# Kernel tuning notes

Measured on AMD Instinct MI355X. Metric: run time of the kernel, lower is better.

The kernel has to match this reference:

```python
import jax, jax.numpy as jnp
import numpy as np
import math

IN_CH = 1024
OUT_CH = 1024
QK_DIM = 512
NHEADS = 8
NDIM = QK_DIM // NHEADS  # 64 per-head qk dim
VDIM = OUT_CH // NHEADS  # 128 per-head value dim
SCALE = 1.0 / math.sqrt(NDIM)


def setup_inputs() -> dict:
    key = jax.random.key(0)
    ks = jax.random.split(key, 7)
    B, N = 4, 2048
    x = jax.random.normal(ks[0], (B, N, IN_CH), dtype=jnp.float32)
    # Linear weights stored as [in, out] so y = x @ W + b
    s_in = 1.0 / math.sqrt(IN_CH)
    Wq = jax.random.uniform(ks[1], (IN_CH, QK_DIM), jnp.float32, -s_in, s_in)
    bq = jax.random.uniform(ks[2], (QK_DIM,), jnp.float32, -s_in, s_in)
    Wk = jax.random.uniform(ks[3], (IN_CH, QK_DIM), jnp.float32, -s_in, s_in)
    bk = jax.random.uniform(ks[4], (QK_DIM,), jnp.float32, -s_in, s_in)
    Wv = jax.random.uniform(ks[5], (IN_CH, OUT_CH), jnp.float32, -s_in, s_in)
    bv = jax.random.uniform(ks[6], (OUT_CH,), jnp.float32, -s_in, s_in)
    return {"x": x, "Wq": Wq, "bq": bq, "Wk": Wk, "bk": bk, "Wv": Wv, "bv": bv}


def reference(x, Wq, bq, Wk, bk, Wv, bv):
    B, N, C = x.shape
    Q = (x @ Wq + bq).reshape(B, N, NHEADS, NDIM)
    K = (x @ Wk + bk).reshape(B, N, NHEADS, NDIM)
    V = (x @ Wv + bv).reshape(B, N, NHEADS, VDIM)
    # scores: [B, H, N, N]
    scores = jnp.einsum("bnhd,bmhd->bhnm", Q, K) * SCALE
    attn = jax.nn.softmax(scores, axis=-1)
    # message: [B, N, H, VDIM] -> [B, N, OUT_CH]
    msg = jnp.einsum("bhnm,bmhv->bnhv", attn, V)
    return msg.reshape(B, N, OUT_CH)
```

## Files before the change

### kernel.cpp

```cpp
#include <hip/hip_runtime.h>
#include <hip/hip_bf16.h>
#include <math.h>


using bf16 = __hip_bfloat16;
typedef __attribute__((ext_vector_type(8))) short short8;
typedef __attribute__((ext_vector_type(4))) float f32x4;
typedef __attribute__((ext_vector_type(16))) float f32x16;
typedef __attribute__((ext_vector_type(2))) unsigned int uintx2;

#define C2 0.18033688011112042f

__device__ __forceinline__ void async_ld16(const void* g, void* l) {
  __builtin_amdgcn_global_load_lds(
      (const __attribute__((address_space(1))) unsigned int*)g,
      (__attribute__((address_space(3))) unsigned int*)l, 16, 0, 0);
}

__global__ __launch_bounds__(256) void convert_x(const float* __restrict__ x,
                                                 bf16* __restrict__ xb)
{
  const int i = (blockIdx.x * 256 + threadIdx.x) * 8;
  const float4 a = *(const float4*)(x + i);
  const float4 b = *(const float4*)(x + i + 4);
  union { bf16 h[8]; short8 s; } u;
  u.h[0] = __float2bfloat16(a.x); u.h[1] = __float2bfloat16(a.y);
  u.h[2] = __float2bfloat16(a.z); u.h[3] = __float2bfloat16(a.w);
  u.h[4] = __float2bfloat16(b.x); u.h[5] = __float2bfloat16(b.y);
  u.h[6] = __float2bfloat16(b.z); u.h[7] = __float2bfloat16(b.w);
  *(short8*)(xb + i) = u.s;
}

__global__ __launch_bounds__(256) void transpose_weights(
    const float* __restrict__ Wq, const float* __restrict__ Wk,
    const float* __restrict__ Wv, bf16* __restrict__ Wt)
{
  __shared__ __align__(16) bf16 t[32][33];
  const int i0 = blockIdx.x * 32;
  const int o0 = blockIdx.y * 32;
  const int tx = threadIdx.x & 31, ty = threadIdx.x >> 5;
#pragma unroll
  for (int s = 0; s < 32; s += 8) {
    const int i = i0 + ty + s;
    const int o = o0 + tx;
    const float w = (o < 512)  ? Wq[(size_t)i * 512 + o]
                  : (o < 1024) ? Wk[(size_t)i * 512 + (o - 512)]
                               : Wv[(size_t)i * 1024 + (o - 1024)];
    t[ty + s][tx] = __float2bfloat16(w);
  }
  __syncthreads();
#pragma unroll
  for (int s = 0; s < 32; s += 8)
    Wt[(size_t)(o0 + ty + s) * 1024 + i0 + tx] = t[tx][ty + s];
}

__global__ __launch_bounds__(256, 2) void qkv_gemm(
    const bf16* __restrict__ xb, const bf16* __restrict__ Wt,
    const float* __restrict__ bq, const float* __restrict__ bk,
    const float* __restrict__ bv, bf16* __restrict__ QKV)
{
  __shared__ __align__(16) bf16 As[128 * 64];
  __shared__ __align__(16) bf16 Bs[128 * 64];
  const int tid = threadIdx.x;
  const int w = tid >> 6, lane = tid & 63, quad = lane >> 4, l16 = lane & 15;
  const int m0 = blockIdx.y * 128, n0 = blockIdx.x * 128;
  const int wm = (w >> 1) * 64, wn = (w & 1) * 64;
  f32x4 acc[4][4];
  const f32x4 z4 = {0.f, 0.f, 0.f, 0.f};
#pragma unroll
  for (int mi = 0; mi < 4; ++mi)
#pragma unroll
    for (int ni = 0; ni < 4; ++ni) acc[mi][ni] = z4;

  for (int k0 = 0; k0 < 1024; k0 += 64) {
    __syncthreads();
#pragma unroll
    for (int it = 0; it < 4; ++it) {
      const int L = it * 256 + tid;
      const int row = L >> 3;
      const int c16 = (L & 7) ^ (row & 7);
      async_ld16(xb + (size_t)(m0 + row) * 1024 + k0 + c16 * 8, &As[L * 8]);
      async_ld16(Wt + (size_t)(n0 + row) * 1024 + k0 + c16 * 8, &Bs[L * 8]);
    }
    __syncthreads();
#pragma unroll
    for (int kk = 0; kk < 2; ++kk) {
      short8 af[4], bfr[4];
#pragma unroll
      for (int mi = 0; mi < 4; ++mi) {
        const int row = wm + mi * 16 + l16;
        const int p = ((kk << 2) | quad) ^ (row & 7);
        af[mi] = *(const short8*)&As[row * 64 + p * 8];
      }
#pragma unroll
      for (int ni = 0; ni < 4; ++ni) {
        const int row = wn + ni * 16 + l16;
        const int p = ((kk << 2) | quad) ^ (row & 7);
        bfr[ni] = *(const short8*)&Bs[row * 64 + p * 8];
      }
#pragma unroll
      for (int mi = 0; mi < 4; ++mi)
#pragma unroll
        for (int ni = 0; ni < 4; ++ni)
          acc[mi][ni] = __builtin_amdgcn_mfma_f32_16x16x32_bf16(af[mi], bfr[ni], acc[mi][ni], 0, 0, 0);
    }
  }
#pragma unroll
  for (int ni = 0; ni < 4; ++ni) {
    const int colg = n0 + wn + ni * 16 + l16;
    const float bias = colg < 512 ? bq[colg]
                     : (colg < 1024 ? bk[colg - 512] : bv[colg - 1024]);
    const float scl = (colg >= 512 && colg < 1024) ? C2 : 1.0f;
#pragma unroll
    for (int mi = 0; mi < 4; ++mi)
#pragma unroll
      for (int reg = 0; reg < 4; ++reg) {
        const int rowg = m0 + wm + mi * 16 + quad * 4 + reg;
        QKV[(size_t)rowg * 2048 + colg] = __float2bfloat16((acc[mi][ni][reg] + bias) * scl);
      }
  }
}

__global__ __launch_bounds__(256) void transpose_v(
    const bf16* __restrict__ QKV, bf16* __restrict__ Vt)
{
  __shared__ __align__(16) bf16 t[32][33];
  const int r0 = blockIdx.x * 32;
  const int c0 = blockIdx.y * 32;
  const int tx = threadIdx.x & 31, ty = threadIdx.x >> 5;
#pragma unroll
  for (int s = 0; s < 32; s += 8)
    t[ty + s][tx] = QKV[(size_t)(r0 + ty + s) * 2048 + 1024 + c0 + tx];
  __syncthreads();
#pragma unroll
  for (int s = 0; s < 32; s += 8)
    Vt[(size_t)(c0 + ty + s) * 8192 + r0 + tx] = t[tx][ty + s];
}

__global__ __launch_bounds__(256, 2) void flash_attn(
    const bf16* __restrict__ QKV, const bf16* __restrict__ Vt, float* __restrict__ out)
{
  __shared__ __align__(16) bf16 smem[3 * 12288];
  char* smemc = (char*)smem;
  const int tid = threadIdx.x;
  const int w = tid >> 6, lane = tid & 63, l31 = lane & 31, hi = lane >> 5;
  const int q0 = blockIdx.x * 128;
  const int h  = blockIdx.y;
  const size_t tb = (size_t)blockIdx.z * 2048;

  short8 qf[4];
  const int qrow = w * 32 + l31;
  const bf16* qptr = QKV + (tb + q0 + qrow) * 2048 + h * 64 + hi * 8;
#pragma unroll
  for (int dd = 0; dd < 4; ++dd)
    qf[dd] = *(const short8*)(qptr + dd * 16);

  int adr[4];
#pragma unroll
  for (int i = 0; i < 4; ++i)
    adr[i] = l31 * 128 + (((2 * i + hi) ^ (l31 & 7)) * 16);

  const bf16* kg[2]; int kldo[2];
#pragma unroll
  for (int i = 0; i < 2; ++i) {
    const int L = i * 256 + tid, row = L >> 3, c = (L & 7) ^ (row & 7);
    kg[i] = QKV + (tb + row) * 2048 + 512 + h * 64 + c * 8;
    kldo[i] = L * 16;
  }
  const bf16* vg[4]; int vldo[4];
#pragma unroll
  for (int i = 0; i < 4; ++i) {
    const int L = i * 256 + tid, row = L >> 3, c = (L & 7) ^ (row & 7);
    vg[i] = Vt + (size_t)(h * 128 + row) * 8192 + tb + c * 8;
    vldo[i] = L * 16;
  }

  f32x16 O[4];
#pragma unroll
  for (int t = 0; t < 4; ++t)
#pragma unroll
    for (int e = 0; e < 16; ++e) O[t][e] = 0.f;
  f32x16 Z;
#pragma unroll
  for (int e = 0; e < 16; ++e) Z[e] = 0.f;
  float2 rs; rs.x = 0.f; rs.y = 0.f;

#define STAGE(B) do {                                                        \
  _Pragma("unroll") for (int i = 0; i < 2; ++i) {                            \
    async_ld16(kg[i], smemc + (B) * 24576 + kldo[i]); kg[i] += 131072; }     \
  _Pragma("unroll") for (int i = 0; i < 4; ++i) {                            \
    async_ld16(vg[i], smemc + (B) * 24576 + 8192 + vldo[i]); vg[i] += 64; }  \
} while (0)

#define SOFTPV(B, KT, SV) do {                                               \
  unsigned int pk[8];                                                        \
  _Pragma("unroll") for (int dw = 0; dw < 8; ++dw) {                         \
    const float e0 = exp2f(SV[2 * dw]);                                      \
    const float e1 = exp2f(SV[2 * dw + 1]);                                  \
    rs.x += e0; rs.y += e1;                                                  \
    union { bf16 hh[2]; unsigned int u; } cc;                                \
    cc.hh[0] = __float2bfloat16(e0); cc.hh[1] = __float2bfloat16(e1);        \
    pk[dw] = cc.u; }                                                         \
  _Pragma("unroll") for (int half = 0; half < 2; ++half) {                   \
    const int kc = 2 * (KT) + half; const int b4 = half * 4;                 \
    const uintx2 s0 = __builtin_amdgcn_permlane32_swap(pk[b4], pk[b4 + 2], false, false);     \
    const uintx2 s1 = __builtin_amdgcn_permlane32_swap(pk[b4 + 1], pk[b4 + 3], false, false); \
    union { unsigned int d[4]; short8 v; } pf;                               \
    pf.d[0] = s0.x; pf.d[1] = s1.x; pf.d[2] = s0.y; pf.d[3] = s1.y;          \
    _Pragma("unroll") for (int vt = 0; vt < 4; ++vt) {                       \
      const short8 vf = *(const short8*)(smemc + (B) * 24576 + 8192 + vt * 4096 + adr[kc]); \
      O[vt] = __builtin_amdgcn_mfma_f32_32x32x16_bf16(vf, pf.v, O[vt], 0, 0, 0); } }        \
} while (0)

#define COMPUTE(B) do {                                                      \
  __builtin_amdgcn_s_setprio(1);                                            \
  short8 kf; f32x16 S0, S1;                                                  \
  kf = *(const short8*)(smemc + (B) * 24576 + adr[0]);                       \
  S0 = __builtin_amdgcn_mfma_f32_32x32x16_bf16(kf, qf[0], Z, 0, 0, 0);       \
  kf = *(const short8*)(smemc + (B) * 24576 + adr[1]);                       \
  S0 = __builtin_amdgcn_mfma_f32_32x32x16_bf16(kf, qf[1], S0, 0, 0, 0);      \
  kf = *(const short8*)(smemc + (B) * 24576 + adr[2]);                       \
  S0 = __builtin_amdgcn_mfma_f32_32x32x16_bf16(kf, qf[2], S0, 0, 0, 0);      \
  kf = *(const short8*)(smemc + (B) * 24576 + adr[3]);                       \
  S0 = __builtin_amdgcn_mfma_f32_32x32x16_bf16(kf, qf[3], S0, 0, 0, 0);      \
  kf = *(const short8*)(smemc + (B) * 24576 + 4096 + adr[0]);                \
  S1 = __builtin_amdgcn_mfma_f32_32x32x16_bf16(kf, qf[0], Z, 0, 0, 0);       \
  kf = *(const short8*)(smemc + (B) * 24576 + 4096 + adr[1]);                \
  S1 = __builtin_amdgcn_mfma_f32_32x32x16_bf16(kf, qf[1], S1, 0, 0, 0);      \
  kf = *(const short8*)(smemc + (B) * 24576 + 4096 + adr[2]);                \
  S1 = __builtin_amdgcn_mfma_f32_32x32x16_bf16(kf, qf[2], S1, 0, 0, 0);      \
  kf = *(const short8*)(smemc + (B) * 24576 + 4096 + adr[3]);                \
  S1 = __builtin_amdgcn_mfma_f32_32x32x16_bf16(kf, qf[3], S1, 0, 0, 0);      \
  SOFTPV(B, 0, S0);                                                          \
  SOFTPV(B, 1, S1);                                                          \
  __builtin_amdgcn_s_setprio(0);                                            \
} while (0)

#define PIPE_SYNC6 do {                                                      \
  asm volatile("s_waitcnt vmcnt(6)" ::: "memory");                           \
  __builtin_amdgcn_s_barrier();                                              \
  __builtin_amdgcn_sched_barrier(0);                                         \
} while (0)

  STAGE(0); STAGE(1);
  PIPE_SYNC6;
  for (int u = 0; u < 10; ++u) {
    STAGE(2); COMPUTE(0); PIPE_SYNC6;
    STAGE(0); COMPUTE(1); PIPE_SYNC6;
    STAGE(1); COMPUTE(2); PIPE_SYNC6;
  }
  COMPUTE(0);
  asm volatile("s_waitcnt vmcnt(0)" ::: "memory");
  __builtin_amdgcn_s_barrier();
  __builtin_amdgcn_sched_barrier(0);
  COMPUTE(1);

#undef STAGE
#undef SOFTPV
#undef COMPUTE
#undef PIPE_SYNC6

  float l_run = rs.x + rs.y;
  l_run += __shfl_xor(l_run, 32, 64);

  const float inv_l = 1.0f / l_run;
  float* tbuf = (float*)smem;
  const int qg = tid >> 1;
  const int part = tid & 1;
  for (int vt = 0; vt < 4; ++vt) {
    __syncthreads();
#pragma unroll
    for (int e = 0; e < 16; ++e) {
      const int vl = (e & 3) + 8 * (e >> 2) + 4 * hi;
      tbuf[vl * 132 + w * 32 + l31] = O[vt][e] * inv_l;
    }
    __syncthreads();
    float* dst = out + (tb + q0 + qg) * 1024 + h * 128 + vt * 32 + part * 16;
#pragma unroll
    for (int i = 0; i < 4; ++i) {
      float4 v4;
      v4.x = tbuf[(part * 16 + 4 * i + 0) * 132 + qg];
      v4.y = tbuf[(part * 16 + 4 * i + 1) * 132 + qg];
      v4.z = tbuf[(part * 16 + 4 * i + 2) * 132 + qg];
      v4.w = tbuf[(part * 16 + 4 * i + 3) * 132 + qg];
      *(float4*)(dst + 4 * i) = v4;
    }
  }
}

extern "C" void kernel_launch(void* const* d_in, const int* in_sizes, int n_in,
                              void* d_out, int out_size, void* d_ws, size_t ws_size,
                              hipStream_t stream) {
  const float* x  = (const float*)d_in[0];
  const float* Wq = (const float*)d_in[1];
  const float* bq = (const float*)d_in[2];
  const float* Wk = (const float*)d_in[3];
  const float* bk = (const float*)d_in[4];
  const float* Wv = (const float*)d_in[5];
  const float* bv = (const float*)d_in[6];
  float* out = (float*)d_out;

  char* ws = (char*)d_ws;
  bf16* QKV = (bf16*)ws;
  bf16* Vt  = (bf16*)(ws + 33554432);
  bf16* Wt  = (bf16*)(ws + 33554432 + 16777216);
  bf16* xb  = (bf16*)(ws + 33554432 + 16777216 + 4194304);

  convert_x<<<dim3(4096), 256, 0, stream>>>(x, xb);
  transpose_weights<<<dim3(32, 64), 256, 0, stream>>>(Wq, Wk, Wv, Wt);
  qkv_gemm<<<dim3(16, 64), 256, 0, stream>>>(xb, Wt, bq, bk, bv, QKV);
  transpose_v<<<dim3(256, 32), 256, 0, stream>>>(QKV, Vt);
  flash_attn<<<dim3(16, 8, 4), 256, 0, stream>>>(QKV, Vt, out);
}
```

Before: 226.9 us.

## Split attention over two key halves with combine pass and leaner LDS pipeline

```diff
diff --git a/kernel.cpp b/kernel.cpp
--- a/kernel.cpp
+++ b/kernel.cpp
@@ -57,7 +57,7 @@
 __global__ __launch_bounds__(256, 2) void qkv_gemm(
     const bf16* __restrict__ xb, const bf16* __restrict__ Wt,
     const float* __restrict__ bq, const float* __restrict__ bk,
-    const float* __restrict__ bv, bf16* __restrict__ QKV)
+    const float* __restrict__ bv, bf16* __restrict__ QK, bf16* __restrict__ Vtmp)
 {
   __shared__ __align__(16) bf16 As[128 * 64];
   __shared__ __align__(16) bf16 Bs[128 * 64];
@@ -105,6 +105,8 @@
           acc[mi][ni] = __builtin_amdgcn_mfma_f32_16x16x32_bf16(af[mi], bfr[ni], acc[mi][ni], 0, 0, 0);
     }
   }
+  bf16* dst = (n0 < 1024) ? QK : Vtmp;
+  const int cofs = (n0 < 1024) ? 0 : 1024;
 #pragma unroll
   for (int ni = 0; ni < 4; ++ni) {
     const int colg = n0 + wn + ni * 16 + l16;
@@ -116,13 +118,13 @@
 #pragma unroll
       for (int reg = 0; reg < 4; ++reg) {
         const int rowg = m0 + wm + mi * 16 + quad * 4 + reg;
-        QKV[(size_t)rowg * 2048 + colg] = __float2bfloat16((acc[mi][ni][reg] + bias) * scl);
+        dst[(size_t)rowg * 1024 + (colg - cofs)] = __float2bfloat16((acc[mi][ni][reg] + bias) * scl);
       }
   }
 }
 
 __global__ __launch_bounds__(256) void transpose_v(
-    const bf16* __restrict__ QKV, bf16* __restrict__ Vt)
+    const bf16* __restrict__ Vtmp, bf16* __restrict__ Vt)
 {
   __shared__ __align__(16) bf16 t[32][33];
   const int r0 = blockIdx.x * 32;
@@ -130,27 +132,32 @@
   const int tx = threadIdx.x & 31, ty = threadIdx.x >> 5;
 #pragma unroll
   for (int s = 0; s < 32; s += 8)
-    t[ty + s][tx] = QKV[(size_t)(r0 + ty + s) * 2048 + 1024 + c0 + tx];
+    t[ty + s][tx] = Vtmp[(size_t)(r0 + ty + s) * 1024 + c0 + tx];
   __syncthreads();
 #pragma unroll
   for (int s = 0; s < 32; s += 8)
     Vt[(size_t)(c0 + ty + s) * 8192 + r0 + tx] = t[tx][ty + s];
 }
 
-__global__ __launch_bounds__(256, 2) void flash_attn(
-    const bf16* __restrict__ QKV, const bf16* __restrict__ Vt, float* __restrict__ out)
-{
-  __shared__ __align__(16) bf16 smem[3 * 12288];
+__global__ __launch_bounds__(256, 4) void flash_attn(
+    const bf16* __restrict__ QK, const bf16* __restrict__ Vt,
+    float* __restrict__ out, float* __restrict__ P1,
+    float* __restrict__ l0, float* __restrict__ l1)
+{
+  __shared__ __align__(16) bf16 smem[16384];
   char* smemc = (char*)smem;
   const int tid = threadIdx.x;
   const int w = tid >> 6, lane = tid & 63, l31 = lane & 31, hi = lane >> 5;
   const int q0 = blockIdx.x * 128;
   const int h  = blockIdx.y;
-  const size_t tb = (size_t)blockIdx.z * 2048;
+  const int b  = blockIdx.z >> 1;
+  const int half_ = blockIdx.z & 1;
+  const int kbase = half_ * 1024;
+  const size_t tb = (size_t)b * 2048;
 
   short8 qf[4];
   const int qrow = w * 32 + l31;
-  const bf16* qptr = QKV + (tb + q0 + qrow) * 2048 + h * 64 + hi * 8;
+  const bf16* qptr = QK + (tb + q0 + qrow) * 1024 + h * 64 + hi * 8;
 #pragma unroll
   for (int dd = 0; dd < 4; ++dd)
     qf[dd] = *(const short8*)(qptr + dd * 16);
@@ -164,16 +171,17 @@
 #pragma unroll
   for (int i = 0; i < 2; ++i) {
     const int L = i * 256 + tid, row = L >> 3, c = (L & 7) ^ (row & 7);
-    kg[i] = QKV + (tb + row) * 2048 + 512 + h * 64 + c * 8;
+    kg[i] = QK + (tb + kbase + row) * 1024 + 512 + h * 64 + c * 8;
     kldo[i] = L * 16;
   }
   const bf16* vg[4]; int vldo[4];
 #pragma unroll
   for (int i = 0; i < 4; ++i) {
     const int L = i * 256 + tid, row = L >> 3, c = (L & 7) ^ (row & 7);
-    vg[i] = Vt + (size_t)(h * 128 + row) * 8192 + tb + c * 8;
+    vg[i] = Vt + (size_t)(h * 128 + row) * 8192 + tb + kbase + c * 8;
     vldo[i] = L * 16;
   }
+  int4 vr[4];
 
   f32x16 O[4];
 #pragma unroll
@@ -185,14 +193,16 @@
   for (int e = 0; e < 16; ++e) Z[e] = 0.f;
   float2 rs; rs.x = 0.f; rs.y = 0.f;
 
-#define STAGE(B) do {                                                        \
-  _Pragma("unroll") for (int i = 0; i < 2; ++i) {                            \
-    async_ld16(kg[i], smemc + (B) * 24576 + kldo[i]); kg[i] += 131072; }     \
-  _Pragma("unroll") for (int i = 0; i < 4; ++i) {                            \
-    async_ld16(vg[i], smemc + (B) * 24576 + 8192 + vldo[i]); vg[i] += 64; }  \
-} while (0)
-
-#define SOFTPV(B, KT, SV) do {                                               \
+#define VLOAD() do { _Pragma("unroll") for (int i = 0; i < 4; ++i) {         \
+    vr[i] = *(const int4*)vg[i]; vg[i] += 64; } } while (0)
+
+#define VSTORE() do { _Pragma("unroll") for (int i = 0; i < 4; ++i)          \
+    *(int4*)(smemc + 16384 + vldo[i]) = vr[i]; } while (0)
+
+#define KSTAGE(PAR) do { _Pragma("unroll") for (int i = 0; i < 2; ++i) {     \
+    async_ld16(kg[i], smemc + (PAR) * 8192 + kldo[i]); kg[i] += 65536; } } while (0)
+
+#define SOFTPV(KT, SV) do {                                                  \
   unsigned int pk[8];                                                        \
   _Pragma("unroll") for (int dw = 0; dw < 8; ++dw) {                         \
     const float e0 = exp2f(SV[2 * dw]);                                      \
@@ -208,62 +218,76 @@
     union { unsigned int d[4]; short8 v; } pf;                               \
     pf.d[0] = s0.x; pf.d[1] = s1.x; pf.d[2] = s0.y; pf.d[3] = s1.y;          \
     _Pragma("unroll") for (int vt = 0; vt < 4; ++vt) {                       \
-      const short8 vf = *(const short8*)(smemc + (B) * 24576 + 8192 + vt * 4096 + adr[kc]); \
-      O[vt] = __builtin_amdgcn_mfma_f32_32x32x16_bf16(vf, pf.v, O[vt], 0, 0, 0); } }        \
+      const short8 vf = *(const short8*)(smemc + 16384 + vt * 4096 + adr[kc]); \
+      O[vt] = __builtin_amdgcn_mfma_f32_32x32x16_bf16(vf, pf.v, O[vt], 0, 0, 0); } } \
 } while (0)
 
-#define COMPUTE(B) do {                                                      \
-  __builtin_amdgcn_s_setprio(1);                                            \
+#define COMPUTE(PAR) do {                                                    \
+  __builtin_amdgcn_s_setprio(1);                                             \
   short8 kf; f32x16 S0, S1;                                                  \
-  kf = *(const short8*)(smemc + (B) * 24576 + adr[0]);                       \
+  kf = *(const short8*)(smemc + (PAR) * 8192 + adr[0]);                      \
   S0 = __builtin_amdgcn_mfma_f32_32x32x16_bf16(kf, qf[0], Z, 0, 0, 0);       \
-  kf = *(const short8*)(smemc + (B) * 24576 + adr[1]);                       \
+  kf = *(const short8*)(smemc + (PAR) * 8192 + adr[1]);                      \
   S0 = __builtin_amdgcn_mfma_f32_32x32x16_bf16(kf, qf[1], S0, 0, 0, 0);      \
-  kf = *(const short8*)(smemc + (B) * 24576 + adr[2]);                       \
+  kf = *(const short8*)(smemc + (PAR) * 8192 + adr[2]);                      \
   S0 = __builtin_amdgcn_mfma_f32_32x32x16_bf16(kf, qf[2], S0, 0, 0, 0);      \
-  kf = *(const short8*)(smemc + (B) * 24576 + adr[3]);                       \
+  kf = *(const short8*)(smemc + (PAR) * 8192 + adr[3]);                      \
   S0 = __builtin_amdgcn_mfma_f32_32x32x16_bf16(kf, qf[3], S0, 0, 0, 0);      \
-  kf = *(const short8*)(smemc + (B) * 24576 + 4096 + adr[0]);                \
+  kf = *(const short8*)(smemc + (PAR) * 8192 + 4096 + adr[0]);               \
   S1 = __builtin_amdgcn_mfma_f32_32x32x16_bf16(kf, qf[0], Z, 0, 0, 0);       \
-  kf = *(const short8*)(smemc + (B) * 24576 + 4096 + adr[1]);                \
+  kf = *(const short8*)(smemc + (PAR) * 8192 + 4096 + adr[1]);               \
   S1 = __builtin_amdgcn_mfma_f32_32x32x16_bf16(kf, qf[1], S1, 0, 0, 0);      \
-  kf = *(const short8*)(smemc + (B) * 24576 + 4096 + adr[2]);                \
+  kf = *(const short8*)(smemc + (PAR) * 8192 + 4096 + adr[2]);               \
   S1 = __builtin_amdgcn_mfma_f32_32x32x16_bf16(kf, qf[2], S1, 0, 0, 0);      \
-  kf = *(const short8*)(smemc + (B) * 24576 + 4096 + adr[3]);                \
+  kf = *(const short8*)(smemc + (PAR) * 8192 + 4096 + adr[3]);               \
   S1 = __builtin_amdgcn_mfma_f32_32x32x16_bf16(kf, qf[3], S1, 0, 0, 0);      \
-  SOFTPV(B, 0, S0);                                                          \
-  SOFTPV(B, 1, S1);                                                          \
-  __builtin_amdgcn_s_setprio(0);                                            \
+  SOFTPV(0, S0);                                                             \
+  SOFTPV(1, S1);                                                             \
+  __builtin_amdgcn_s_setprio(0);                                             \
 } while (0)
 
-#define PIPE_SYNC6 do {                                                      \
-  asm volatile("s_waitcnt vmcnt(6)" ::: "memory");                           \
+#define ITER(PAR, DO_STAGE) do {                                             \
+  COMPUTE(PAR);                                                              \
+  asm volatile("s_waitcnt vmcnt(0) lgkmcnt(0)" ::: "memory");                \
+  __builtin_amdgcn_s_barrier();                                              \
+  VSTORE();                                                                  \
+  if (DO_STAGE) { VLOAD(); KSTAGE(PAR); }                                    \
+  asm volatile("s_waitcnt lgkmcnt(0)" ::: "memory");                         \
   __builtin_amdgcn_s_barrier();                                              \
   __builtin_amdgcn_sched_barrier(0);                                         \
 } while (0)
 
-  STAGE(0); STAGE(1);
-  PIPE_SYNC6;
-  for (int u = 0; u < 10; ++u) {
-    STAGE(2); COMPUTE(0); PIPE_SYNC6;
-    STAGE(0); COMPUTE(1); PIPE_SYNC6;
-    STAGE(1); COMPUTE(2); PIPE_SYNC6;
-  }
-  COMPUTE(0);
+  VLOAD();
+  KSTAGE(0);
   asm volatile("s_waitcnt vmcnt(0)" ::: "memory");
+  VSTORE();
+  VLOAD();
+  KSTAGE(1);
+  asm volatile("s_waitcnt lgkmcnt(0)" ::: "memory");
   __builtin_amdgcn_s_barrier();
   __builtin_amdgcn_sched_barrier(0);
+
+  for (int u = 0; u < 7; ++u) {
+    ITER(0, true);
+    ITER(1, true);
+  }
+  ITER(0, false);
   COMPUTE(1);
 
-#undef STAGE
+#undef VLOAD
+#undef VSTORE
+#undef KSTAGE
 #undef SOFTPV
 #undef COMPUTE
-#undef PIPE_SYNC6
+#undef ITER
 
   float l_run = rs.x + rs.y;
   l_run += __shfl_xor(l_run, 32, 64);
-
-  const float inv_l = 1.0f / l_run;
+  float* lx = half_ ? l1 : l0;
+  if (hi == 0)
+    lx[((size_t)b * 8 + h) * 2048 + q0 + w * 32 + l31] = l_run;
+
+  float* Pdst = half_ ? P1 : out;
   float* tbuf = (float*)smem;
   const int qg = tid >> 1;
   const int part = tid & 1;
@@ -272,10 +296,10 @@
 #pragma unroll
     for (int e = 0; e < 16; ++e) {
       const int vl = (e & 3) + 8 * (e >> 2) + 4 * hi;
-      tbuf[vl * 132 + w * 32 + l31] = O[vt][e] * inv_l;
+      tbuf[vl * 132 + w * 32 + l31] = O[vt][e];
     }
     __syncthreads();
-    float* dst = out + (tb + q0 + qg) * 1024 + h * 128 + vt * 32 + part * 16;
+    float* dst = Pdst + (tb + q0 + qg) * 1024 + h * 128 + vt * 32 + part * 16;
 #pragma unroll
     for (int i = 0; i < 4; ++i) {
       float4 v4;
@@ -286,6 +310,26 @@
       *(float4*)(dst + 4 * i) = v4;
     }
   }
+}
+
+__global__ __launch_bounds__(256) void combine(
+    const float* __restrict__ P1, const float* __restrict__ l0,
+    const float* __restrict__ l1, float* out)
+{
+  const size_t i4 = (size_t)blockIdx.x * 256 + threadIdx.x;
+  const size_t e = i4 * 4;
+  const int b = (int)(e >> 21);
+  const int q = (int)(e >> 10) & 2047;
+  const int hh = (int)(e >> 7) & 7;
+  const size_t li = ((size_t)b * 8 + hh) * 2048 + q;
+  const float inv = 1.0f / (l0[li] + l1[li]);
+  float4 a = ((const float4*)out)[i4];
+  const float4 c = ((const float4*)P1)[i4];
+  a.x = (a.x + c.x) * inv;
+  a.y = (a.y + c.y) * inv;
+  a.z = (a.z + c.z) * inv;
+  a.w = (a.w + c.w) * inv;
+  ((float4*)out)[i4] = a;
 }
 
 extern "C" void kernel_launch(void* const* d_in, const int* in_sizes, int n_in,
@@ -301,14 +345,19 @@
   float* out = (float*)d_out;
 
   char* ws = (char*)d_ws;
-  bf16* QKV = (bf16*)ws;
-  bf16* Vt  = (bf16*)(ws + 33554432);
-  bf16* Wt  = (bf16*)(ws + 33554432 + 16777216);
-  bf16* xb  = (bf16*)(ws + 33554432 + 16777216 + 4194304);
+  bf16* QK   = (bf16*)ws;
+  bf16* Vt   = (bf16*)(ws + (16u << 20));
+  bf16* Vtmp = (bf16*)(ws + (32u << 20));
+  bf16* xb   = (bf16*)(ws + (48u << 20));
+  bf16* Wt   = (bf16*)(ws + (64u << 20));
+  float* P1  = (float*)(ws + (32u << 20));
+  float* l0  = (float*)(ws + (64u << 20));
+  float* l1  = (float*)(ws + (64u << 20) + (256u << 10));
 
   convert_x<<<dim3(4096), 256, 0, stream>>>(x, xb);
   transpose_weights<<<dim3(32, 64), 256, 0, stream>>>(Wq, Wk, Wv, Wt);
-  qkv_gemm<<<dim3(16, 64), 256, 0, stream>>>(xb, Wt, bq, bk, bv, QKV);
-  transpose_v<<<dim3(256, 32), 256, 0, stream>>>(QKV, Vt);
-  flash_attn<<<dim3(16, 8, 4), 256, 0, stream>>>(QKV, Vt, out);
-}
+  qkv_gemm<<<dim3(16, 64), 256, 0, stream>>>(xb, Wt, bq, bk, bv, QK, Vtmp);
+  transpose_v<<<dim3(256, 32), 256, 0, stream>>>(Vtmp, Vt);
+  flash_attn<<<dim3(16, 8, 8), 256, 0, stream>>>(QK, Vt, out, P1, l0, l1);
+  combine<<<dim3(8192), 256, 0, stream>>>(P1, l0, l1, out);
+}
```

Result: slower. 422.0 us (+86.0%).

## Double-buffer QKV GEMM loads and write transposed V directly from epilogue

Applied to the files above, without the earlier changes.

```diff
diff --git a/kernel.cpp b/kernel.cpp
--- a/kernel.cpp
+++ b/kernel.cpp
@@ -4,6 +4,7 @@
 
 
 using bf16 = __hip_bfloat16;
+typedef __attribute__((ext_vector_type(4))) short bf16x4;
 typedef __attribute__((ext_vector_type(8))) short short8;
 typedef __attribute__((ext_vector_type(4))) float f32x4;
 typedef __attribute__((ext_vector_type(16))) float f32x16;
@@ -57,14 +58,21 @@
 __global__ __launch_bounds__(256, 2) void qkv_gemm(
     const bf16* __restrict__ xb, const bf16* __restrict__ Wt,
     const float* __restrict__ bq, const float* __restrict__ bk,
-    const float* __restrict__ bv, bf16* __restrict__ QKV)
+    const float* __restrict__ bv, bf16* __restrict__ QKV, bf16* __restrict__ Vt)
 {
-  __shared__ __align__(16) bf16 As[128 * 64];
-  __shared__ __align__(16) bf16 Bs[128 * 64];
+  __shared__ __align__(16) bf16 As[2][8192];
+  __shared__ __align__(16) bf16 Bs[2][8192];
   const int tid = threadIdx.x;
   const int w = tid >> 6, lane = tid & 63, quad = lane >> 4, l16 = lane & 15;
   const int m0 = blockIdx.y * 128, n0 = blockIdx.x * 128;
   const int wm = (w >> 1) * 64, wn = (w & 1) * 64;
+
+  const int srow = tid >> 3;
+  const int sc   = (tid & 7) ^ (srow & 7);
+  const bf16* xg = xb + (size_t)(m0 + srow) * 1024 + sc * 8;
+  const bf16* wg = Wt + (size_t)(n0 + srow) * 1024 + sc * 8;
+  const int ldb = tid * 16;
+
   f32x4 acc[4][4];
   const f32x4 z4 = {0.f, 0.f, 0.f, 0.f};
 #pragma unroll
@@ -72,69 +80,97 @@
 #pragma unroll
     for (int ni = 0; ni < 4; ++ni) acc[mi][ni] = z4;
 
-  for (int k0 = 0; k0 < 1024; k0 += 64) {
-    __syncthreads();
-#pragma unroll
-    for (int it = 0; it < 4; ++it) {
-      const int L = it * 256 + tid;
-      const int row = L >> 3;
-      const int c16 = (L & 7) ^ (row & 7);
-      async_ld16(xb + (size_t)(m0 + row) * 1024 + k0 + c16 * 8, &As[L * 8]);
-      async_ld16(Wt + (size_t)(n0 + row) * 1024 + k0 + c16 * 8, &Bs[L * 8]);
+#define QSTAGE(BUF) do {                                                     \
+  async_ld16(xg,         (char*)As[BUF] + ldb);                              \
+  async_ld16(xg + 32768, (char*)As[BUF] + ldb + 4096);                       \
+  async_ld16(xg + 65536, (char*)As[BUF] + ldb + 8192);                       \
+  async_ld16(xg + 98304, (char*)As[BUF] + ldb + 12288);                      \
+  async_ld16(wg,         (char*)Bs[BUF] + ldb);                              \
+  async_ld16(wg + 32768, (char*)Bs[BUF] + ldb + 4096);                       \
+  async_ld16(wg + 65536, (char*)Bs[BUF] + ldb + 8192);                       \
+  async_ld16(wg + 98304, (char*)Bs[BUF] + ldb + 12288);                      \
+  xg += 64; wg += 64;                                                        \
+} while (0)
+
+#define QCOMP(BUF) do {                                                      \
+  _Pragma("unroll") for (int kk = 0; kk < 2; ++kk) {                         \
+    short8 af[4], bfr[4];                                                    \
+    _Pragma("unroll") for (int mi = 0; mi < 4; ++mi) {                       \
+      const int row = wm + mi * 16 + l16;                                    \
+      const int p = ((kk << 2) | quad) ^ (row & 7);                          \
+      af[mi] = *(const short8*)&As[BUF][row * 64 + p * 8];                   \
+    }                                                                        \
+    _Pragma("unroll") for (int ni = 0; ni < 4; ++ni) {                       \
+      const int row = wn + ni * 16 + l16;                                    \
+      const int p = ((kk << 2) | quad) ^ (row & 7);                          \
+      bfr[ni] = *(const short8*)&Bs[BUF][row * 64 + p * 8];                  \
+    }                                                                        \
+    _Pragma("unroll") for (int mi = 0; mi < 4; ++mi)                         \
+      _Pragma("unroll") for (int ni = 0; ni < 4; ++ni)                       \
+        acc[mi][ni] = __builtin_amdgcn_mfma_f32_16x16x32_bf16(af[mi], bfr[ni], acc[mi][ni], 0, 0, 0); \
+  }                                                                          \
+} while (0)
+
+#define QBODY(BUF, DO_STAGE) do {                                            \
+  if (DO_STAGE) {                                                            \
+    QSTAGE((BUF) ^ 1);                                                       \
+    asm volatile("s_waitcnt vmcnt(8)" ::: "memory");                         \
+  } else {                                                                   \
+    asm volatile("s_waitcnt vmcnt(0)" ::: "memory");                         \
+  }                                                                          \
+  __builtin_amdgcn_s_barrier();                                              \
+  __builtin_amdgcn_sched_barrier(0);                                         \
+  QCOMP(BUF);                                                                \
+  asm volatile("s_waitcnt lgkmcnt(0)" ::: "memory");                         \
+  __builtin_amdgcn_s_barrier();                                              \
+  __builtin_amdgcn_sched_barrier(0);                                         \
+} while (0)
+
+  QSTAGE(0);
+  for (int u = 0; u < 7; ++u) {
+    QBODY(0, true);
+    QBODY(1, true);
+  }
+  QBODY(0, true);
+  asm volatile("s_waitcnt vmcnt(0)" ::: "memory");
+  __builtin_amdgcn_s_barrier();
+  __builtin_amdgcn_sched_barrier(0);
+  QCOMP(1);
+
+#undef QSTAGE
+#undef QCOMP
+#undef QBODY
+
+  if (n0 < 1024) {
+#pragma unroll
+    for (int ni = 0; ni < 4; ++ni) {
+      const int colg = n0 + wn + ni * 16 + l16;
+      const float bias = colg < 512 ? bq[colg] : bk[colg - 512];
+      const float scl = (colg >= 512) ? C2 : 1.0f;
+#pragma unroll
+      for (int mi = 0; mi < 4; ++mi)
+#pragma unroll
+        for (int reg = 0; reg < 4; ++reg) {
+          const int rowg = m0 + wm + mi * 16 + quad * 4 + reg;
+          QKV[(size_t)rowg * 2048 + colg] = __float2bfloat16((acc[mi][ni][reg] + bias) * scl);
+        }
     }
-    __syncthreads();
-#pragma unroll
-    for (int kk = 0; kk < 2; ++kk) {
-      short8 af[4], bfr[4];
+  } else {
+#pragma unroll
+    for (int ni = 0; ni < 4; ++ni) {
+      const int v = n0 - 1024 + wn + ni * 16 + l16;
+      const float bias = bv[v];
 #pragma unroll
       for (int mi = 0; mi < 4; ++mi) {
-        const int row = wm + mi * 16 + l16;
-        const int p = ((kk << 2) | quad) ^ (row & 7);
-        af[mi] = *(const short8*)&As[row * 64 + p * 8];
+        const int rowg0 = m0 + wm + mi * 16 + quad * 4;
+        union { bf16 h[4]; bf16x4 s; } u;
+#pragma unroll
+        for (int reg = 0; reg < 4; ++reg)
+          u.h[reg] = __float2bfloat16(acc[mi][ni][reg] + bias);
+        *(bf16x4*)(Vt + (size_t)v * 8192 + rowg0) = u.s;
       }
-#pragma unroll
-      for (int ni = 0; ni < 4; ++ni) {
-        const int row = wn + ni * 16 + l16;
-        const int p = ((kk << 2) | quad) ^ (row & 7);
-        bfr[ni] = *(const short8*)&Bs[row * 64 + p * 8];
-      }
-#pragma unroll
-      for (int mi = 0; mi < 4; ++mi)
-#pragma unroll
-        for (int ni = 0; ni < 4; ++ni)
-          acc[mi][ni] = __builtin_amdgcn_mfma_f32_16x16x32_bf16(af[mi], bfr[ni], acc[mi][ni], 0, 0, 0);
     }
   }
-#pragma unroll
-  for (int ni = 0; ni < 4; ++ni) {
-    const int colg = n0 + wn + ni * 16 + l16;
-    const float bias = colg < 512 ? bq[colg]
-                     : (colg < 1024 ? bk[colg - 512] : bv[colg - 1024]);
-    const float scl = (colg >= 512 && colg < 1024) ? C2 : 1.0f;
-#pragma unroll
-    for (int mi = 0; mi < 4; ++mi)
-#pragma unroll
-      for (int reg = 0; reg < 4; ++reg) {
-        const int rowg = m0 + wm + mi * 16 + quad * 4 + reg;
-        QKV[(size_t)rowg * 2048 + colg] = __float2bfloat16((acc[mi][ni][reg] + bias) * scl);
-      }
-  }
-}
-
-__global__ __launch_bounds__(256) void transpose_v(
-    const bf16* __restrict__ QKV, bf16* __restrict__ Vt)
-{
-  __shared__ __align__(16) bf16 t[32][33];
-  const int r0 = blockIdx.x * 32;
-  const int c0 = blockIdx.y * 32;
-  const int tx = threadIdx.x & 31, ty = threadIdx.x >> 5;
-#pragma unroll
-  for (int s = 0; s < 32; s += 8)
-    t[ty + s][tx] = QKV[(size_t)(r0 + ty + s) * 2048 + 1024 + c0 + tx];
-  __syncthreads();
-#pragma unroll
-  for (int s = 0; s < 32; s += 8)
-    Vt[(size_t)(c0 + ty + s) * 8192 + r0 + tx] = t[tx][ty + s];
 }
 
 __global__ __launch_bounds__(256, 2) void flash_attn(
@@ -308,7 +344,6 @@
 
   convert_x<<<dim3(4096), 256, 0, stream>>>(x, xb);
   transpose_weights<<<dim3(32, 64), 256, 0, stream>>>(Wq, Wk, Wv, Wt);
-  qkv_gemm<<<dim3(16, 64), 256, 0, stream>>>(xb, Wt, bq, bk, bv, QKV);
-  transpose_v<<<dim3(256, 32), 256, 0, stream>>>(QKV, Vt);
+  qkv_gemm<<<dim3(16, 64), 256, 0, stream>>>(xb, Wt, bq, bk, bv, QKV, Vt);
   flash_attn<<<dim3(16, 8, 4), 256, 0, stream>>>(QKV, Vt, out);
 }
```

Result: faster. 212.6 us (-6.3%).
